# Kernel tuning notes

Measured on AMD Instinct MI355X. Metric: run time of the kernel, lower is better.

Reference implementation:

```python
import jax, jax.numpy as jnp
import numpy as np


def setup_inputs() -> dict:
    key = jax.random.key(0)
    kE, kD, kW, kU, kV = jax.random.split(key, 5)
    B, T, H, U = 32, 2048, 1024, 1024
    scale = 0.02
    return {
        "enc_out": jax.random.normal(kE, (B, T, H), dtype=jnp.float32),
        "dec_hidden": jax.random.normal(kD, (B, H), dtype=jnp.float32),
        "Wa": jax.random.normal(kW, (H, U), dtype=jnp.float32) * scale,
        "Ua": jax.random.normal(kU, (H, U), dtype=jnp.float32) * scale,
        "Va": jax.random.normal(kV, (U,), dtype=jnp.float32) * scale,
    }


def reference(enc_out, dec_hidden, Wa, Ua, Va):
    # Bahdanau additive attention.
    # enc_out: [B, T, H]; dec_hidden: [B, H]; Wa: [H, U]; Ua: [H, U]; Va: [U]
    dec_proj = jnp.einsum("bh,hu->bu", dec_hidden, Wa)          # [B, U]
    enc_proj = jnp.einsum("bth,hu->btu", enc_out, Ua)            # [B, T, U]
    s = jnp.tanh(enc_proj + dec_proj[:, None, :])                # [B, T, U]
    score = jnp.einsum("btu,u->bt", s, Va)                       # [B, T]
    alpha = jax.nn.softmax(score, axis=-1)                       # [B, T]
    context = jnp.einsum("bt,bth->bh", alpha, enc_out)           # [B, H]
    return context
```

## Files before the change

kernel.cpp:

```cpp
#include <hip/hip_runtime.h>
#include <stdint.h>


#define B_ 32
#define T_ 2048
#define H_ 1024
#define U_ 1024
#define M_ (B_ * T_)

typedef __bf16 bf16x8 __attribute__((ext_vector_type(8)));
typedef float f32x4 __attribute__((ext_vector_type(4)));

__device__ __forceinline__ unsigned f2b(float f) {
  unsigned u = __float_as_uint(f);
  return (u + 0x7FFFu + ((u >> 16) & 1u)) >> 16;
}
__device__ __forceinline__ float b2f(unsigned short u) {
  return __uint_as_float(((unsigned)u) << 16);
}
__device__ __forceinline__ float fast_tanh(float x) {
  float xc = fminf(fmaxf(x, -12.f), 12.f);
  float t = exp2f(xc * 2.885390081777927f);
  return (t - 1.f) * __builtin_amdgcn_rcpf(t + 1.f);
}

#define AS1 __attribute__((address_space(1)))
#define AS3 __attribute__((address_space(3)))
__device__ __forceinline__ void gld_lds16(const void* g, void* l) {
  __builtin_amdgcn_global_load_lds((AS1 const void*)g, (AS3 void*)l, 16, 0, 0);
}

__global__ __launch_bounds__(256) void conv_enc_k(const float4* __restrict__ in,
                                                  uint4* __restrict__ outA) {
  __shared__ uint4 L4[128 * 17];
  const int tx = threadIdx.x;
  const int band = blockIdx.x;
  const int mt = band >> 3;
  const int R = (band & 7) << 4;
  const float4* src = in + (size_t)band * 4096;
#pragma unroll
  for (int i = 0; i < 8; ++i) {
    int p = i * 256 + tx;
    int r = p >> 7, pc = p & 127;
    float4 a = src[r * 256 + pc * 2];
    float4 b = src[r * 256 + pc * 2 + 1];
    uint4 o;
    o.x = f2b(a.x) | (f2b(a.y) << 16);
    o.y = f2b(a.z) | (f2b(a.w) << 16);
    o.z = f2b(b.x) | (f2b(b.y) << 16);
    o.w = f2b(b.z) | (f2b(b.w) << 16);
    L4[pc * 17 + r] = o;
  }
  __syncthreads();
  const int r2 = tx & 15, kq = (tx >> 4) & 3, w = tx >> 6;
#pragma unroll
  for (int j = 0; j < 8; ++j) {
    int k8 = j * 16 + w * 4 + kq;
    outA[((size_t)mt * 128 + k8) * 128 + R + r2] = L4[k8 * 17 + r2];
  }
}

__global__ __launch_bounds__(256) void conv_ua_k(const float* __restrict__ in,
                                                 uint4* __restrict__ out) {
  int id = blockIdx.x * 256 + threadIdx.x;
  int h8 = id >> 10, u = id & 1023;
  const float* p = in + (size_t)(h8 << 3) * U_ + u;
  uint4 o;
  o.x = f2b(p[0]) | (f2b(p[U_]) << 16);
  o.y = f2b(p[2 * U_]) | (f2b(p[3 * U_]) << 16);
  o.z = f2b(p[4 * U_]) | (f2b(p[5 * U_]) << 16);
  o.w = f2b(p[6 * U_]) | (f2b(p[7 * U_]) << 16);
  out[(size_t)h8 * U_ + u] = o;
}

__global__ __launch_bounds__(256) void decproj_k(const float* __restrict__ dh,
                                                 const float* __restrict__ Wa,
                                                 float* __restrict__ dp4) {
  const int u = blockIdx.x * 256 + threadIdx.x;
  const int b = blockIdx.y, hz = blockIdx.z;
  const float* d = dh + b * H_ + hz * 256;
  const float* w = Wa + (size_t)(hz * 256) * U_ + u;
  float a0 = 0.f, a1 = 0.f, a2 = 0.f, a3 = 0.f;
#pragma unroll 4
  for (int h = 0; h < 256; h += 4) {
    a0 = fmaf(d[h + 0], w[(size_t)(h + 0) * U_], a0);
    a1 = fmaf(d[h + 1], w[(size_t)(h + 1) * U_], a1);
    a2 = fmaf(d[h + 2], w[(size_t)(h + 2) * U_], a2);
    a3 = fmaf(d[h + 3], w[(size_t)(h + 3) * U_], a3);
  }
  dp4[((hz * B_ + b) * U_) + u] = (a0 + a1) + (a2 + a3);
}

__global__ __launch_bounds__(256, 2) void score_gemm_k(
    const unsigned short* __restrict__ encA,
    const unsigned short* __restrict__ Ub,
    const float* __restrict__ dp4,
    const float* __restrict__ Va,
    float* __restrict__ score8)
{
  __shared__ union {
    struct {
      alignas(16) unsigned short As[8][128][8];
      alignas(16) unsigned short Bs[8][128][8];
    } t;
    float sred[128 * 33];
  } sm;

  const int bx = blockIdx.x;
  const int mtile = ((bx >> 6) << 3) | (bx & 7), ntile = (bx >> 3) & 7;
  const int m0 = mtile << 7, n0 = ntile << 7;
  const int tid = threadIdx.x;
  const int wv = tid >> 6, ln = tid & 63;
  const int wm = wv & 1, wn = wv >> 1;
  const int quad = ln >> 4, l16 = ln & 15;

  f32x4 acc[4][4];
  const f32x4 zero = {0.f, 0.f, 0.f, 0.f};
#pragma unroll
  for (int i = 0; i < 4; ++i)
#pragma unroll
    for (int j = 0; j < 4; ++j) acc[i][j] = zero;

  const unsigned short* encT = encA + (size_t)mtile * (128 * 128 * 8);

  for (int k0 = 0; k0 < H_; k0 += 64) {
    __syncthreads();
#pragma unroll
    for (int c = 0; c < 4; ++c) {
      int chunk = (wv << 2) + c;
      int k8 = chunk >> 1, half = chunk & 1;
      const unsigned short* ga =
          encT + (((size_t)((k0 >> 3) + k8) * 128) + (half << 6) + ln) * 8;
      gld_lds16(ga, &sm.t.As[k8][half << 6][0]);
      const unsigned short* gb =
          Ub + (((size_t)((k0 >> 3) + k8) * U_) + n0 + (half << 6) + ln) * 8;
      gld_lds16(gb, &sm.t.Bs[k8][half << 6][0]);
    }
    __syncthreads();

#pragma unroll
    for (int kk = 0; kk < 2; ++kk) {
      int k8b = (kk << 2) + quad;
      bf16x8 af[4], bf[4];
#pragma unroll
      for (int mt = 0; mt < 4; ++mt)
        af[mt] = *(const bf16x8*)&sm.t.As[k8b][(wm << 6) + (mt << 4) + l16][0];
#pragma unroll
      for (int nt = 0; nt < 4; ++nt)
        bf[nt] = *(const bf16x8*)&sm.t.Bs[k8b][(wn << 6) + (nt << 4) + l16][0];
#pragma unroll
      for (int mt = 0; mt < 4; ++mt)
#pragma unroll
        for (int nt = 0; nt < 4; ++nt)
          acc[mt][nt] = __builtin_amdgcn_mfma_f32_16x16x32_bf16(
              af[mt], bf[nt], acc[mt][nt], 0, 0, 0);
    }
  }

  const int bq = m0 >> 11;
  float va[4], dpv[4];
#pragma unroll
  for (int nt = 0; nt < 4; ++nt) {
    int col = n0 + (wn << 6) + (nt << 4) + l16;
    va[nt] = Va[col];
    dpv[nt] = dp4[bq * U_ + col] + dp4[B_ * U_ + bq * U_ + col] +
              dp4[2 * B_ * U_ + bq * U_ + col] + dp4[3 * B_ * U_ + bq * U_ + col];
  }
  __syncthreads();
#pragma unroll
  for (int mt = 0; mt < 4; ++mt) {
#pragma unroll
    for (int r = 0; r < 4; ++r) {
      float v = 0.f;
#pragma unroll
      for (int nt = 0; nt < 4; ++nt)
        v += fast_tanh(acc[mt][nt][r] + dpv[nt]) * va[nt];
      int row = (wm << 6) + (mt << 4) + (quad << 2) + r;
      sm.sred[row * 33 + (wn << 4) + l16] = v;
    }
  }
  __syncthreads();
  if (tid < 128) {
    const float* p = &sm.sred[tid * 33];
    float s = 0.f;
#pragma unroll
    for (int j = 0; j < 32; ++j) s += p[j];
    score8[(size_t)ntile * M_ + m0 + tid] = s;
  }
}

__global__ __launch_bounds__(256) void softmax_k(const float* __restrict__ score8,
                                                 float* __restrict__ alpha) {
  const int b = blockIdx.x, tid = threadIdx.x;
  __shared__ float red[4];
  float4 v0 = {0.f, 0.f, 0.f, 0.f}, v1 = {0.f, 0.f, 0.f, 0.f};
#pragma unroll
  for (int k = 0; k < 8; ++k) {
    const float4* p = (const float4*)(score8 + (size_t)k * M_ + b * T_);
    float4 x0 = p[tid * 2], x1 = p[tid * 2 + 1];
    v0.x += x0.x; v0.y += x0.y; v0.z += x0.z; v0.w += x0.w;
    v1.x += x1.x; v1.y += x1.y; v1.z += x1.z; v1.w += x1.w;
  }
  float m = fmaxf(fmaxf(fmaxf(v0.x, v0.y), fmaxf(v0.z, v0.w)),
                  fmaxf(fmaxf(v1.x, v1.y), fmaxf(v1.z, v1.w)));
#pragma unroll
  for (int off = 32; off >= 1; off >>= 1) m = fmaxf(m, __shfl_xor(m, off));
  if ((tid & 63) == 0) red[tid >> 6] = m;
  __syncthreads();
  m = fmaxf(fmaxf(red[0], red[1]), fmaxf(red[2], red[3]));
  __syncthreads();
  const float l2e = 1.4426950408889634f;
  float e[8];
  e[0] = exp2f((v0.x - m) * l2e); e[1] = exp2f((v0.y - m) * l2e);
  e[2] = exp2f((v0.z - m) * l2e); e[3] = exp2f((v0.w - m) * l2e);
  e[4] = exp2f((v1.x - m) * l2e); e[5] = exp2f((v1.y - m) * l2e);
  e[6] = exp2f((v1.z - m) * l2e); e[7] = exp2f((v1.w - m) * l2e);
  float sum = (e[0] + e[1]) + (e[2] + e[3]) + (e[4] + e[5]) + (e[6] + e[7]);
#pragma unroll
  for (int off = 32; off >= 1; off >>= 1) sum += __shfl_xor(sum, off);
  if ((tid & 63) == 0) red[tid >> 6] = sum;
  __syncthreads();
  float inv = 1.f / (red[0] + red[1] + red[2] + red[3]);
  float4* a4 = (float4*)(alpha + b * T_);
  float4 o0, o1;
  o0.x = e[0] * inv; o0.y = e[1] * inv; o0.z = e[2] * inv; o0.w = e[3] * inv;
  o1.x = e[4] * inv; o1.y = e[5] * inv; o1.z = e[6] * inv; o1.w = e[7] * inv;
  a4[tid * 2] = o0;
  a4[tid * 2 + 1] = o1;
}

__global__ __launch_bounds__(256) void context_k(const uint4* __restrict__ encA,
                                                 const float* __restrict__ alpha,
                                                 float* __restrict__ ctxp) {
  const int tx = threadIdx.x & 127, th = threadIdx.x >> 7;
  const int b = blockIdx.y, bt = blockIdx.x;
  const int mt = b * 16 + bt;
  const uint4* base = encA + ((size_t)mt * 128 + tx) * 128 + th * 64;
  const float* al = alpha + b * T_ + bt * 128 + th * 64;
  float a[8];
#pragma unroll
  for (int j = 0; j < 8; ++j) a[j] = 0.f;
#pragma unroll 4
  for (int i = 0; i < 64; ++i) {
    float w = al[i];
    uint4 e = base[i];
    a[0] = fmaf(w, b2f((unsigned short)e.x), a[0]);
    a[1] = fmaf(w, b2f((unsigned short)(e.x >> 16)), a[1]);
    a[2] = fmaf(w, b2f((unsigned short)e.y), a[2]);
    a[3] = fmaf(w, b2f((unsigned short)(e.y >> 16)), a[3]);
    a[4] = fmaf(w, b2f((unsigned short)e.z), a[4]);
    a[5] = fmaf(w, b2f((unsigned short)(e.z >> 16)), a[5]);
    a[6] = fmaf(w, b2f((unsigned short)e.w), a[6]);
    a[7] = fmaf(w, b2f((unsigned short)(e.w >> 16)), a[7]);
  }
  __shared__ float cred[2][128][8];
#pragma unroll
  for (int j = 0; j < 8; ++j) cred[th][tx][j] = a[j];
  __syncthreads();
  if (th == 0) {
    float* o = ctxp + (size_t)mt * H_ + tx * 8;
#pragma unroll
    for (int j = 0; j < 8; ++j) o[j] = cred[0][tx][j] + cred[1][tx][j];
  }
}

__global__ __launch_bounds__(256) void ctx_red_k(const float* __restrict__ ctxp,
                                                 float* __restrict__ out) {
  int id = blockIdx.x * 256 + threadIdx.x;
  int b = id >> 10, h = id & 1023;
  float s = 0.f;
#pragma unroll
  for (int bt = 0; bt < 16; ++bt) s += ctxp[((size_t)(b * 16 + bt)) * H_ + h];
  out[id] = s;
}

extern "C" void kernel_launch(void* const* d_in, const int* in_sizes, int n_in,
                              void* d_out, int out_size, void* d_ws, size_t ws_size,
                              hipStream_t stream) {
  const float* enc = (const float*)d_in[0];
  const float* dh  = (const float*)d_in[1];
  const float* Wa  = (const float*)d_in[2];
  const float* Ua  = (const float*)d_in[3];
  const float* Va  = (const float*)d_in[4];

  char* ws = (char*)d_ws;
  unsigned short* encA = (unsigned short*)ws;
  unsigned short* Ub   = (unsigned short*)(ws + 134217728);
  float* dp4    = (float*)(ws + 136314880);
  float* score8 = (float*)(ws + 136839168);
  float* alpha  = dp4;
  float* ctxp   = score8;

  conv_enc_k<<<4096, 256, 0, stream>>>((const float4*)enc, (uint4*)encA);
  conv_ua_k<<<512, 256, 0, stream>>>(Ua, (uint4*)Ub);
  decproj_k<<<dim3(4, 32, 4), 256, 0, stream>>>(dh, Wa, dp4);
  score_gemm_k<<<4096, 256, 0, stream>>>(encA, Ub, dp4, Va, score8);
  softmax_k<<<32, 256, 0, stream>>>(score8, alpha);
  context_k<<<dim3(16, 32), 256, 0, stream>>>((const uint4*)encA, alpha, ctxp);
  ctx_red_k<<<128, 256, 0, stream>>>(ctxp, (float*)d_out);
}
```

Before: 559.2 us.

## Enlarge score GEMM tile to 256x256 with double-buffered LDS pipelining

The fused score GEMM moves from 128x128 tiles with 256 threads to 256x256 tiles with 512 threads (8 waves). It double-buffers LDS and issues the next k-tile's global-to-LDS loads in four phases interleaved with MFMA work, using explicit waitcnt, scheduling barriers and s_setprio. The epilogue reduction now uses shuffles and writes 4 partial score planes instead of 8, and softmax is updated to match. The goals are more data reuse per tile and hiding load latency, at the cost of more LDS (64KB), higher register pressure and a fragile hand-placed vmcnt count.

```diff
diff --git a/kernel.cpp b/kernel.cpp
--- a/kernel.cpp
+++ b/kernel.cpp
@@ -28,6 +28,12 @@
 #define AS3 __attribute__((address_space(3)))
 __device__ __forceinline__ void gld_lds16(const void* g, void* l) {
   __builtin_amdgcn_global_load_lds((AS1 const void*)g, (AS3 void*)l, 16, 0, 0);
+}
+
+__device__ __forceinline__ void BAR() {
+  __builtin_amdgcn_sched_barrier(0);
+  __builtin_amdgcn_s_barrier();
+  __builtin_amdgcn_sched_barrier(0);
 }
 
 __global__ __launch_bounds__(256) void conv_enc_k(const float4* __restrict__ in,
@@ -91,112 +97,166 @@
   dp4[((hz * B_ + b) * U_) + u] = (a0 + a1) + (a2 + a3);
 }
 
-__global__ __launch_bounds__(256, 2) void score_gemm_k(
+__global__ __launch_bounds__(512, 2) void score_gemm_k(
     const unsigned short* __restrict__ encA,
     const unsigned short* __restrict__ Ub,
     const float* __restrict__ dp4,
     const float* __restrict__ Va,
-    float* __restrict__ score8)
+    float* __restrict__ score4)
 {
   __shared__ union {
     struct {
-      alignas(16) unsigned short As[8][128][8];
-      alignas(16) unsigned short Bs[8][128][8];
+      alignas(16) unsigned short As[2][8][256][8];
+      alignas(16) unsigned short Bs[2][8][256][8];
     } t;
-    float sred[128 * 33];
+    float sred[256][4];
   } sm;
 
   const int bx = blockIdx.x;
-  const int mtile = ((bx >> 6) << 3) | (bx & 7), ntile = (bx >> 3) & 7;
-  const int m0 = mtile << 7, n0 = ntile << 7;
+  const int x = bx & 7, gsl = (bx >> 3) & 3, s = bx >> 5;
+  const int mt2 = s * 8 + x, nt2 = gsl;
+  const int n0 = nt2 << 8;
   const int tid = threadIdx.x;
   const int wv = tid >> 6, ln = tid & 63;
-  const int wm = wv & 1, wn = wv >> 1;
+  const int wm = wv >> 2, wn = wv & 3;
   const int quad = ln >> 4, l16 = ln & 15;
 
-  f32x4 acc[4][4];
+  const unsigned short* encT = encA + (size_t)mt2 * (2 * 128 * 128 * 8);
+
+  auto STAGE = [&](int kt, int hf, int bsel) {
+#pragma unroll
+    for (int r = 0; r < 2; ++r) {
+      int c = r * 8 + wv;
+      int k8 = c >> 1, rg = (c & 1) << 6;
+      if (hf < 2) {
+        const unsigned short* ga =
+            encT + (((size_t)(hf * 128 + kt * 8 + k8) * 128) + rg + ln) * 8;
+        gld_lds16(ga, &sm.t.As[bsel][k8][hf * 128 + rg][0]);
+      } else {
+        int h2 = hf - 2;
+        const unsigned short* gb =
+            Ub + (((size_t)(kt * 8 + k8) * U_) + n0 + h2 * 128 + rg + ln) * 8;
+        gld_lds16(gb, &sm.t.Bs[bsel][k8][h2 * 128 + rg][0]);
+      }
+    }
+  };
+
+  f32x4 acc[8][4];
   const f32x4 zero = {0.f, 0.f, 0.f, 0.f};
 #pragma unroll
-  for (int i = 0; i < 4; ++i)
+  for (int i = 0; i < 8; ++i)
 #pragma unroll
     for (int j = 0; j < 4; ++j) acc[i][j] = zero;
 
-  const unsigned short* encT = encA + (size_t)mtile * (128 * 128 * 8);
-
-  for (int k0 = 0; k0 < H_; k0 += 64) {
-    __syncthreads();
-#pragma unroll
-    for (int c = 0; c < 4; ++c) {
-      int chunk = (wv << 2) + c;
-      int k8 = chunk >> 1, half = chunk & 1;
-      const unsigned short* ga =
-          encT + (((size_t)((k0 >> 3) + k8) * 128) + (half << 6) + ln) * 8;
-      gld_lds16(ga, &sm.t.As[k8][half << 6][0]);
-      const unsigned short* gb =
-          Ub + (((size_t)((k0 >> 3) + k8) * U_) + n0 + (half << 6) + ln) * 8;
-      gld_lds16(gb, &sm.t.Bs[k8][half << 6][0]);
-    }
-    __syncthreads();
-
-#pragma unroll
-    for (int kk = 0; kk < 2; ++kk) {
-      int k8b = (kk << 2) + quad;
-      bf16x8 af[4], bf[4];
-#pragma unroll
-      for (int mt = 0; mt < 4; ++mt)
-        af[mt] = *(const bf16x8*)&sm.t.As[k8b][(wm << 6) + (mt << 4) + l16][0];
-#pragma unroll
-      for (int nt = 0; nt < 4; ++nt)
-        bf[nt] = *(const bf16x8*)&sm.t.Bs[k8b][(wn << 6) + (nt << 4) + l16][0];
-#pragma unroll
-      for (int mt = 0; mt < 4; ++mt)
-#pragma unroll
-        for (int nt = 0; nt < 4; ++nt)
-          acc[mt][nt] = __builtin_amdgcn_mfma_f32_16x16x32_bf16(
-              af[mt], bf[nt], acc[mt][nt], 0, 0, 0);
-    }
-  }
-
-  const int bq = m0 >> 11;
+#pragma unroll
+  for (int hf = 0; hf < 4; ++hf) STAGE(0, hf, 0);
+
+  bf16x8 bfr[4][2];
+
+#pragma unroll 2
+  for (int kt = 0; kt < 16; ++kt) {
+    const int cb = kt & 1, nb = cb ^ 1;
+
+    if (kt < 15) {
+      STAGE(kt + 1, 0, nb);
+      asm volatile("s_waitcnt vmcnt(2)" ::: "memory");
+    } else {
+      asm volatile("s_waitcnt vmcnt(0)" ::: "memory");
+    }
+    BAR();
+#pragma unroll
+    for (int nt = 0; nt < 4; ++nt)
+#pragma unroll
+      for (int kk = 0; kk < 2; ++kk)
+        bfr[nt][kk] = *(const bf16x8*)&sm.t
+                           .Bs[cb][kk * 4 + quad][wn * 64 + nt * 16 + l16][0];
+    {
+      bf16x8 af[2][2];
+#pragma unroll
+      for (int i = 0; i < 2; ++i)
+#pragma unroll
+        for (int kk = 0; kk < 2; ++kk)
+          af[i][kk] = *(const bf16x8*)&sm.t
+                           .As[cb][kk * 4 + quad][wm * 128 + i * 16 + l16][0];
+      __builtin_amdgcn_s_setprio(1);
+#pragma unroll
+      for (int kk = 0; kk < 2; ++kk)
+#pragma unroll
+        for (int i = 0; i < 2; ++i)
+#pragma unroll
+          for (int nt = 0; nt < 4; ++nt)
+            acc[i][nt] = __builtin_amdgcn_mfma_f32_16x16x32_bf16(
+                af[i][kk], bfr[nt][kk], acc[i][nt], 0, 0, 0);
+      __builtin_amdgcn_s_setprio(0);
+    }
+    BAR();
+
+#pragma unroll
+    for (int p = 1; p < 4; ++p) {
+      if (kt < 15) STAGE(kt + 1, p, nb);
+      bf16x8 af[2][2];
+#pragma unroll
+      for (int i = 0; i < 2; ++i)
+#pragma unroll
+        for (int kk = 0; kk < 2; ++kk)
+          af[i][kk] =
+              *(const bf16x8*)&sm.t.As[cb][kk * 4 + quad]
+                                      [wm * 128 + (p * 2 + i) * 16 + l16][0];
+      __builtin_amdgcn_s_setprio(1);
+#pragma unroll
+      for (int kk = 0; kk < 2; ++kk)
+#pragma unroll
+        for (int i = 0; i < 2; ++i)
+#pragma unroll
+          for (int nt = 0; nt < 4; ++nt)
+            acc[p * 2 + i][nt] = __builtin_amdgcn_mfma_f32_16x16x32_bf16(
+                af[i][kk], bfr[nt][kk], acc[p * 2 + i][nt], 0, 0, 0);
+      __builtin_amdgcn_s_setprio(0);
+      BAR();
+    }
+  }
+
+  const int bq = mt2 >> 3;
   float va[4], dpv[4];
 #pragma unroll
-  for (int nt = 0; nt < 4; ++nt) {
-    int col = n0 + (wn << 6) + (nt << 4) + l16;
-    va[nt] = Va[col];
-    dpv[nt] = dp4[bq * U_ + col] + dp4[B_ * U_ + bq * U_ + col] +
-              dp4[2 * B_ * U_ + bq * U_ + col] + dp4[3 * B_ * U_ + bq * U_ + col];
-  }
-  __syncthreads();
-#pragma unroll
-  for (int mt = 0; mt < 4; ++mt) {
-#pragma unroll
-    for (int r = 0; r < 4; ++r) {
+  for (int fn = 0; fn < 4; ++fn) {
+    int col = n0 + wn * 64 + fn * 16 + l16;
+    va[fn] = Va[col];
+    dpv[fn] = dp4[bq * U_ + col] + dp4[B_ * U_ + bq * U_ + col] +
+              dp4[2 * B_ * U_ + bq * U_ + col] +
+              dp4[3 * B_ * U_ + bq * U_ + col];
+  }
+  asm volatile("s_waitcnt vmcnt(0) lgkmcnt(0)" ::: "memory");
+  BAR();
+#pragma unroll
+  for (int fm = 0; fm < 8; ++fm) {
+#pragma unroll
+    for (int rr = 0; rr < 4; ++rr) {
       float v = 0.f;
 #pragma unroll
-      for (int nt = 0; nt < 4; ++nt)
-        v += fast_tanh(acc[mt][nt][r] + dpv[nt]) * va[nt];
-      int row = (wm << 6) + (mt << 4) + (quad << 2) + r;
-      sm.sred[row * 33 + (wn << 4) + l16] = v;
-    }
-  }
-  __syncthreads();
-  if (tid < 128) {
-    const float* p = &sm.sred[tid * 33];
-    float s = 0.f;
-#pragma unroll
-    for (int j = 0; j < 32; ++j) s += p[j];
-    score8[(size_t)ntile * M_ + m0 + tid] = s;
-  }
-}
-
-__global__ __launch_bounds__(256) void softmax_k(const float* __restrict__ score8,
+      for (int fn = 0; fn < 4; ++fn)
+        v += fast_tanh(acc[fm][fn][rr] + dpv[fn]) * va[fn];
+#pragma unroll
+      for (int off = 1; off < 16; off <<= 1) v += __shfl_xor(v, off);
+      if (l16 == 0) sm.sred[wm * 128 + fm * 16 + quad * 4 + rr][wn] = v;
+    }
+  }
+  BAR();
+  if (tid < 256) {
+    float ssum = sm.sred[tid][0] + sm.sred[tid][1] + sm.sred[tid][2] +
+                 sm.sred[tid][3];
+    score4[(size_t)nt2 * M_ + mt2 * 256 + tid] = ssum;
+  }
+}
+
+__global__ __launch_bounds__(256) void softmax_k(const float* __restrict__ score4,
                                                  float* __restrict__ alpha) {
   const int b = blockIdx.x, tid = threadIdx.x;
   __shared__ float red[4];
   float4 v0 = {0.f, 0.f, 0.f, 0.f}, v1 = {0.f, 0.f, 0.f, 0.f};
 #pragma unroll
-  for (int k = 0; k < 8; ++k) {
-    const float4* p = (const float4*)(score8 + (size_t)k * M_ + b * T_);
+  for (int k = 0; k < 4; ++k) {
+    const float4* p = (const float4*)(score4 + (size_t)k * M_ + b * T_);
     float4 x0 = p[tid * 2], x1 = p[tid * 2 + 1];
     v0.x += x0.x; v0.y += x0.y; v0.z += x0.z; v0.w += x0.w;
     v1.x += x1.x; v1.y += x1.y; v1.z += x1.z; v1.w += x1.w;
@@ -287,15 +347,15 @@
   unsigned short* encA = (unsigned short*)ws;
   unsigned short* Ub   = (unsigned short*)(ws + 134217728);
   float* dp4    = (float*)(ws + 136314880);
-  float* score8 = (float*)(ws + 136839168);
+  float* score4 = (float*)(ws + 136839168);
   float* alpha  = dp4;
-  float* ctxp   = score8;
+  float* ctxp   = score4;
 
   conv_enc_k<<<4096, 256, 0, stream>>>((const float4*)enc, (uint4*)encA);
   conv_ua_k<<<512, 256, 0, stream>>>(Ua, (uint4*)Ub);
   decproj_k<<<dim3(4, 32, 4), 256, 0, stream>>>(dh, Wa, dp4);
-  score_gemm_k<<<4096, 256, 0, stream>>>(encA, Ub, dp4, Va, score8);
-  softmax_k<<<32, 256, 0, stream>>>(score8, alpha);
+  score_gemm_k<<<1024, 512, 0, stream>>>(encA, Ub, dp4, Va, score4);
+  softmax_k<<<32, 256, 0, stream>>>(score4, alpha);
   context_k<<<dim3(16, 32), 256, 0, stream>>>((const uint4*)encA, alpha, ctxp);
   ctx_red_k<<<128, 256, 0, stream>>>(ctxp, (float*)d_out);
 }
```

New measurement: 566.7 us. No clear change (+1.3%).

## Fuse prep kernels into one launch and fold softmax and reduction into context

Applied to the files above, without the earlier changes.

The encoder conversion, Ua conversion, decoder projection and output zeroing now run as block ranges of a single prep kernel. Softmax, context accumulation and the final cross-tile reduction are merged into one context kernel. Each block recomputes the softmax statistics for its batch row and adds its partial context into the output with atomicAdd. This removes four kernel launches and the alpha and ctxp round-trips through global memory, at the cost of redundant softmax work per block and atomic contention on the output.

```diff
diff --git a/kernel.cpp b/kernel.cpp
--- a/kernel.cpp
+++ b/kernel.cpp
@@ -30,65 +30,68 @@
   __builtin_amdgcn_global_load_lds((AS1 const void*)g, (AS3 void*)l, 16, 0, 0);
 }
 
-__global__ __launch_bounds__(256) void conv_enc_k(const float4* __restrict__ in,
-                                                  uint4* __restrict__ outA) {
-  __shared__ uint4 L4[128 * 17];
+__global__ __launch_bounds__(256) void prep_k(
+    const float4* __restrict__ enc, uint4* __restrict__ outA,
+    const float* __restrict__ Ua, uint4* __restrict__ Ub,
+    const float* __restrict__ dh, const float* __restrict__ Wa,
+    float* __restrict__ dp4, float* __restrict__ outz) {
+  const int bx = blockIdx.x;
   const int tx = threadIdx.x;
-  const int band = blockIdx.x;
-  const int mt = band >> 3;
-  const int R = (band & 7) << 4;
-  const float4* src = in + (size_t)band * 4096;
-#pragma unroll
-  for (int i = 0; i < 8; ++i) {
-    int p = i * 256 + tx;
-    int r = p >> 7, pc = p & 127;
-    float4 a = src[r * 256 + pc * 2];
-    float4 b = src[r * 256 + pc * 2 + 1];
+
+  if (bx < 4096) {
+    __shared__ uint4 L4[128 * 17];
+    const int band = bx;
+    const int mt = band >> 3;
+    const int R = (band & 7) << 4;
+    const float4* src = enc + (size_t)band * 4096;
+#pragma unroll
+    for (int i = 0; i < 8; ++i) {
+      int p = i * 256 + tx;
+      int r = p >> 7, pc = p & 127;
+      float4 a = src[r * 256 + pc * 2];
+      float4 b = src[r * 256 + pc * 2 + 1];
+      uint4 o;
+      o.x = f2b(a.x) | (f2b(a.y) << 16);
+      o.y = f2b(a.z) | (f2b(a.w) << 16);
+      o.z = f2b(b.x) | (f2b(b.y) << 16);
+      o.w = f2b(b.z) | (f2b(b.w) << 16);
+      L4[pc * 17 + r] = o;
+    }
+    __syncthreads();
+    const int r2 = tx & 15, kq = (tx >> 4) & 3, w = tx >> 6;
+#pragma unroll
+    for (int j = 0; j < 8; ++j) {
+      int k8 = j * 16 + w * 4 + kq;
+      outA[((size_t)mt * 128 + k8) * 128 + R + r2] = L4[k8 * 17 + r2];
+    }
+  } else if (bx < 4608) {
+    int id = (bx - 4096) * 256 + tx;
+    int h8 = id >> 10, u = id & 1023;
+    const float* p = Ua + (size_t)(h8 << 3) * U_ + u;
     uint4 o;
-    o.x = f2b(a.x) | (f2b(a.y) << 16);
-    o.y = f2b(a.z) | (f2b(a.w) << 16);
-    o.z = f2b(b.x) | (f2b(b.y) << 16);
-    o.w = f2b(b.z) | (f2b(b.w) << 16);
-    L4[pc * 17 + r] = o;
-  }
-  __syncthreads();
-  const int r2 = tx & 15, kq = (tx >> 4) & 3, w = tx >> 6;
-#pragma unroll
-  for (int j = 0; j < 8; ++j) {
-    int k8 = j * 16 + w * 4 + kq;
-    outA[((size_t)mt * 128 + k8) * 128 + R + r2] = L4[k8 * 17 + r2];
-  }
-}
-
-__global__ __launch_bounds__(256) void conv_ua_k(const float* __restrict__ in,
-                                                 uint4* __restrict__ out) {
-  int id = blockIdx.x * 256 + threadIdx.x;
-  int h8 = id >> 10, u = id & 1023;
-  const float* p = in + (size_t)(h8 << 3) * U_ + u;
-  uint4 o;
-  o.x = f2b(p[0]) | (f2b(p[U_]) << 16);
-  o.y = f2b(p[2 * U_]) | (f2b(p[3 * U_]) << 16);
-  o.z = f2b(p[4 * U_]) | (f2b(p[5 * U_]) << 16);
-  o.w = f2b(p[6 * U_]) | (f2b(p[7 * U_]) << 16);
-  out[(size_t)h8 * U_ + u] = o;
-}
-
-__global__ __launch_bounds__(256) void decproj_k(const float* __restrict__ dh,
-                                                 const float* __restrict__ Wa,
-                                                 float* __restrict__ dp4) {
-  const int u = blockIdx.x * 256 + threadIdx.x;
-  const int b = blockIdx.y, hz = blockIdx.z;
-  const float* d = dh + b * H_ + hz * 256;
-  const float* w = Wa + (size_t)(hz * 256) * U_ + u;
-  float a0 = 0.f, a1 = 0.f, a2 = 0.f, a3 = 0.f;
+    o.x = f2b(p[0]) | (f2b(p[U_]) << 16);
+    o.y = f2b(p[2 * U_]) | (f2b(p[3 * U_]) << 16);
+    o.z = f2b(p[4 * U_]) | (f2b(p[5 * U_]) << 16);
+    o.w = f2b(p[6 * U_]) | (f2b(p[7 * U_]) << 16);
+    Ub[(size_t)h8 * U_ + u] = o;
+  } else if (bx < 5120) {
+    int g = bx - 4608;
+    const int u = (g & 3) * 256 + tx;
+    const int b = (g >> 2) & 31, hz = g >> 7;
+    const float* d = dh + b * H_ + hz * 256;
+    const float* w = Wa + (size_t)(hz * 256) * U_ + u;
+    float a0 = 0.f, a1 = 0.f, a2 = 0.f, a3 = 0.f;
 #pragma unroll 4
-  for (int h = 0; h < 256; h += 4) {
-    a0 = fmaf(d[h + 0], w[(size_t)(h + 0) * U_], a0);
-    a1 = fmaf(d[h + 1], w[(size_t)(h + 1) * U_], a1);
-    a2 = fmaf(d[h + 2], w[(size_t)(h + 2) * U_], a2);
-    a3 = fmaf(d[h + 3], w[(size_t)(h + 3) * U_], a3);
-  }
-  dp4[((hz * B_ + b) * U_) + u] = (a0 + a1) + (a2 + a3);
+    for (int h = 0; h < 256; h += 4) {
+      a0 = fmaf(d[h + 0], w[(size_t)(h + 0) * U_], a0);
+      a1 = fmaf(d[h + 1], w[(size_t)(h + 1) * U_], a1);
+      a2 = fmaf(d[h + 2], w[(size_t)(h + 2) * U_], a2);
+      a3 = fmaf(d[h + 3], w[(size_t)(h + 3) * U_], a3);
+    }
+    dp4[((hz * B_ + b) * U_) + u] = (a0 + a1) + (a2 + a3);
+  } else {
+    outz[(bx - 5120) * 256 + tx] = 0.f;
+  }
 }
 
 __global__ __launch_bounds__(256, 2) void score_gemm_k(
@@ -189,10 +192,15 @@
   }
 }
 
-__global__ __launch_bounds__(256) void softmax_k(const float* __restrict__ score8,
-                                                 float* __restrict__ alpha) {
-  const int b = blockIdx.x, tid = threadIdx.x;
+__global__ __launch_bounds__(256) void ctx_k(const uint4* __restrict__ encA,
+                                             const float* __restrict__ score8,
+                                             float* __restrict__ out) {
+  const int b = blockIdx.y, bt = blockIdx.x, tid = threadIdx.x;
+  __shared__ float s_sc[2048];
+  __shared__ float a_s[128];
   __shared__ float red[4];
+  __shared__ float cred[2][128][8];
+
   float4 v0 = {0.f, 0.f, 0.f, 0.f}, v1 = {0.f, 0.f, 0.f, 0.f};
 #pragma unroll
   for (int k = 0; k < 8; ++k) {
@@ -201,6 +209,9 @@
     v0.x += x0.x; v0.y += x0.y; v0.z += x0.z; v0.w += x0.w;
     v1.x += x1.x; v1.y += x1.y; v1.z += x1.z; v1.w += x1.w;
   }
+  ((float4*)s_sc)[tid * 2] = v0;
+  ((float4*)s_sc)[tid * 2 + 1] = v1;
+
   float m = fmaxf(fmaxf(fmaxf(v0.x, v0.y), fmaxf(v0.z, v0.w)),
                   fmaxf(fmaxf(v1.x, v1.y), fmaxf(v1.z, v1.w)));
 #pragma unroll
@@ -209,40 +220,30 @@
   __syncthreads();
   m = fmaxf(fmaxf(red[0], red[1]), fmaxf(red[2], red[3]));
   __syncthreads();
+
   const float l2e = 1.4426950408889634f;
-  float e[8];
-  e[0] = exp2f((v0.x - m) * l2e); e[1] = exp2f((v0.y - m) * l2e);
-  e[2] = exp2f((v0.z - m) * l2e); e[3] = exp2f((v0.w - m) * l2e);
-  e[4] = exp2f((v1.x - m) * l2e); e[5] = exp2f((v1.y - m) * l2e);
-  e[6] = exp2f((v1.z - m) * l2e); e[7] = exp2f((v1.w - m) * l2e);
-  float sum = (e[0] + e[1]) + (e[2] + e[3]) + (e[4] + e[5]) + (e[6] + e[7]);
+  float sum = exp2f((v0.x - m) * l2e) + exp2f((v0.y - m) * l2e) +
+              exp2f((v0.z - m) * l2e) + exp2f((v0.w - m) * l2e) +
+              exp2f((v1.x - m) * l2e) + exp2f((v1.y - m) * l2e) +
+              exp2f((v1.z - m) * l2e) + exp2f((v1.w - m) * l2e);
 #pragma unroll
   for (int off = 32; off >= 1; off >>= 1) sum += __shfl_xor(sum, off);
   if ((tid & 63) == 0) red[tid >> 6] = sum;
   __syncthreads();
-  float inv = 1.f / (red[0] + red[1] + red[2] + red[3]);
-  float4* a4 = (float4*)(alpha + b * T_);
-  float4 o0, o1;
-  o0.x = e[0] * inv; o0.y = e[1] * inv; o0.z = e[2] * inv; o0.w = e[3] * inv;
-  o1.x = e[4] * inv; o1.y = e[5] * inv; o1.z = e[6] * inv; o1.w = e[7] * inv;
-  a4[tid * 2] = o0;
-  a4[tid * 2 + 1] = o1;
-}
-
-__global__ __launch_bounds__(256) void context_k(const uint4* __restrict__ encA,
-                                                 const float* __restrict__ alpha,
-                                                 float* __restrict__ ctxp) {
-  const int tx = threadIdx.x & 127, th = threadIdx.x >> 7;
-  const int b = blockIdx.y, bt = blockIdx.x;
+  const float inv = 1.f / (red[0] + red[1] + red[2] + red[3]);
+
+  if (tid < 128) a_s[tid] = exp2f((s_sc[bt * 128 + tid] - m) * l2e) * inv;
+  __syncthreads();
+
+  const int tx = tid & 127, th = tid >> 7;
   const int mt = b * 16 + bt;
   const uint4* base = encA + ((size_t)mt * 128 + tx) * 128 + th * 64;
-  const float* al = alpha + b * T_ + bt * 128 + th * 64;
   float a[8];
 #pragma unroll
   for (int j = 0; j < 8; ++j) a[j] = 0.f;
 #pragma unroll 4
   for (int i = 0; i < 64; ++i) {
-    float w = al[i];
+    float w = a_s[th * 64 + i];
     uint4 e = base[i];
     a[0] = fmaf(w, b2f((unsigned short)e.x), a[0]);
     a[1] = fmaf(w, b2f((unsigned short)(e.x >> 16)), a[1]);
@@ -253,25 +254,15 @@
     a[6] = fmaf(w, b2f((unsigned short)e.w), a[6]);
     a[7] = fmaf(w, b2f((unsigned short)(e.w >> 16)), a[7]);
   }
-  __shared__ float cred[2][128][8];
 #pragma unroll
   for (int j = 0; j < 8; ++j) cred[th][tx][j] = a[j];
   __syncthreads();
   if (th == 0) {
-    float* o = ctxp + (size_t)mt * H_ + tx * 8;
-#pragma unroll
-    for (int j = 0; j < 8; ++j) o[j] = cred[0][tx][j] + cred[1][tx][j];
-  }
-}
-
-__global__ __launch_bounds__(256) void ctx_red_k(const float* __restrict__ ctxp,
-                                                 float* __restrict__ out) {
-  int id = blockIdx.x * 256 + threadIdx.x;
-  int b = id >> 10, h = id & 1023;
-  float s = 0.f;
-#pragma unroll
-  for (int bt = 0; bt < 16; ++bt) s += ctxp[((size_t)(b * 16 + bt)) * H_ + h];
-  out[id] = s;
+    float* o = out + (size_t)b * H_ + tx * 8;
+#pragma unroll
+    for (int j = 0; j < 8; ++j)
+      atomicAdd(&o[j], cred[0][tx][j] + cred[1][tx][j]);
+  }
 }
 
 extern "C" void kernel_launch(void* const* d_in, const int* in_sizes, int n_in,
@@ -288,14 +279,10 @@
   unsigned short* Ub   = (unsigned short*)(ws + 134217728);
   float* dp4    = (float*)(ws + 136314880);
   float* score8 = (float*)(ws + 136839168);
-  float* alpha  = dp4;
-  float* ctxp   = score8;
-
-  conv_enc_k<<<4096, 256, 0, stream>>>((const float4*)enc, (uint4*)encA);
-  conv_ua_k<<<512, 256, 0, stream>>>(Ua, (uint4*)Ub);
-  decproj_k<<<dim3(4, 32, 4), 256, 0, stream>>>(dh, Wa, dp4);
+
+  prep_k<<<5248, 256, 0, stream>>>((const float4*)enc, (uint4*)encA, Ua,
+                                   (uint4*)Ub, dh, Wa, dp4, (float*)d_out);
   score_gemm_k<<<4096, 256, 0, stream>>>(encA, Ub, dp4, Va, score8);
-  softmax_k<<<32, 256, 0, stream>>>(score8, alpha);
-  context_k<<<dim3(16, 32), 256, 0, stream>>>((const uint4*)encA, alpha, ctxp);
-  ctx_red_k<<<128, 256, 0, stream>>>(ctxp, (float*)d_out);
-}
+  ctx_k<<<dim3(16, 32), 256, 0, stream>>>((const uint4*)encA, score8,
+                                          (float*)d_out);
+}
```

After: 562.1 us. No clear change (+0.5%).
